# Kernel optimization log

Measured on AMD Instinct MI355X. Metric: run time of the kernel, lower is better.

## Reference

```python
import jax, jax.numpy as jnp
import numpy as np

NEG_SLOPE = 0.02

def setup_inputs() -> dict:
    key = jax.random.key(0)
    ks = jax.random.split(key, 6)
    B, C, H, W = 32, 64, 128, 128
    K, L, OUT = 1000, 12, 24
    x = jax.random.normal(ks[0], (B, C, H, W), dtype=jnp.float32)
    pos = jax.random.randint(ks[1], (K, B, L, 2), 0, 128, dtype=jnp.int32)
    # middle: Conv2d(C, C, 3, stride=1, padding=1)
    conv_w = jax.random.normal(ks[2], (C, C, 3, 3), dtype=jnp.float32) * (1.0 / np.sqrt(C * 9))
    conv_b = jax.random.normal(ks[3], (C,), dtype=jnp.float32) * 0.01
    # predictor: Linear(C*L, OUT), kaiming init, zero bias
    pred_w = jax.random.normal(ks[4], (OUT, C * L), dtype=jnp.float32) * np.sqrt(2.0 / (C * L))
    pred_b = jnp.zeros((OUT,), dtype=jnp.float32)
    return {"x": x, "pos": pos, "conv_w": conv_w, "conv_b": conv_b, "pred_w": pred_w, "pred_b": pred_b}

def reference(x, pos, conv_w, conv_b, pred_w, pred_b):
    # middle conv (3x3, same padding) + LeakyReLU(0.02)
    h = jax.lax.conv_general_dilated(
        x, conv_w, window_strides=(1, 1), padding=((1, 1), (1, 1)),
        dimension_numbers=("NCHW", "OIHW", "NCHW")) + conv_b[None, :, None, None]
    h = jnp.where(h > 0, h, NEG_SLOPE * h)  # [B,C,H,W]
    B, C, H, W = h.shape
    K, _, L, _ = pos.shape
    # clamp coords and build flattened spatial indices
    px = jnp.clip(pos[..., 0], 0, W - 1)
    py = jnp.clip(pos[..., 1], 0, H - 1)
    idx = (py * W + px).transpose(1, 0, 2)           # [B,K,L]
    hf = h.reshape(B, C, H * W).transpose(0, 2, 1)   # [B,HW,C]
    # irregular gather: per-batch pick L spatial locations for K candidates
    kernel_seq = hf[jnp.arange(B)[:, None, None], idx]  # [B,K,L,C]
    kernel_seq = kernel_seq.reshape(B, K, L * C)
    out = kernel_seq @ pred_w.T + pred_b             # [B,K,OUT]
    return out.transpose(1, 0, 2)                    # [K,B,OUT]
```

## Files before the change

kernel.cpp:

```cpp
#include <hip/hip_runtime.h>
#include <hip/hip_bf16.h>

typedef __attribute__((ext_vector_type(8))) short short8;
typedef __attribute__((ext_vector_type(4))) float f32x4;

#define NEG_SLOPE 0.02f

static __device__ __forceinline__ unsigned short f2bf(float f) {
    unsigned int u = __float_as_uint(f);
    u += 0x7fffu + ((u >> 16) & 1u);
    return (unsigned short)(u >> 16);
}

static __device__ __forceinline__ unsigned int pk2bf(float lo, float hi) {
    __hip_bfloat162 t = __float22bfloat162_rn(float2{lo, hi});
    unsigned int u;
    __builtin_memcpy(&u, &t, 4);
    return u;
}

__global__ __launch_bounds__(256) void prep_kernel(const float* __restrict__ conv_w,
                                                   const float* __restrict__ pred_w,
                                                   unsigned short* __restrict__ wb,
                                                   unsigned short* __restrict__ pwb) {
    int i = blockIdx.x * 256 + threadIdx.x;
    if (i < 36864) {
        int ci5 = i & 31, tap = (i >> 5) % 9, rest = i / 288;
        int co = rest & 63, cc = rest >> 6;
        int ci = cc * 32 + ci5;
        wb[i] = f2bf(conv_w[(co * 64 + ci) * 9 + tap]);
    }
    if (i < 24576) {
        int o = i / 768, k = i - o * 768;
        pwb[i] = f2bf(o < 24 ? pred_w[o * 768 + k] : 0.0f);
    }
}

#define ROW_BYTES 8320
#define WROW 304
__global__ __launch_bounds__(512, 4) void conv_mfma(const float* __restrict__ x,
                                                    const unsigned short* __restrict__ wb,
                                                    const float* __restrict__ cb,
                                                    unsigned short* __restrict__ h) {
    __shared__ unsigned short w_sm[64 * WROW];
    __shared__ unsigned char in_sm[4 * ROW_BYTES];

    const int id = blockIdx.x;
    const int xcd = id & 7, local = id >> 3;
    const int b = local & 31;
    const int y0 = ((xcd << 3) + (local >> 5)) * 2;

    const int tid = threadIdx.x;
    const int wave = tid >> 6, lane = tid & 63;
    const int lr = lane & 15, kg = lane >> 4;
    const int ro = wave >> 2;
    const int px0 = (wave & 3) * 32;

    f32x4 acc[2][4];
#pragma unroll
    for (int m = 0; m < 2; ++m)
#pragma unroll
        for (int n = 0; n < 4; ++n) acc[m][n] = (f32x4){0.f, 0.f, 0.f, 0.f};

    const unsigned char* ab[2][3];
#pragma unroll
    for (int m = 0; m < 2; ++m)
#pragma unroll
        for (int dx = 0; dx < 3; ++dx) {
            int xx = px0 + m * 16 + lr + dx;
            int pair = xx >> 1, odd = xx & 1;
            int slot = ((odd << 2) | kg) ^ (pair & 7);
            ab[m][dx] = in_sm + pair * 128 + slot * 16;
        }
    const unsigned short* bbp[4];
#pragma unroll
    for (int n = 0; n < 4; ++n) bbp[n] = w_sm + (n * 16 + lr) * WROW + kg * 8;

    const int s_pair = wave * 8 + (lane >> 3);
    const int s_odd = (lane >> 2) & 1, s_q = lane & 3;
    const int s_xx = s_pair * 2 + s_odd;
    const int s_gx = s_xx - 1;
    const int s_gxc = s_gx < 0 ? 0 : s_gx;
    const int s_slot = ((s_odd << 2) | s_q) ^ (s_pair & 7);
    const int s_dst = s_pair * 128 + s_slot * 16;

    for (int cc = 0; cc < 2; ++cc) {
        __syncthreads();
        const unsigned short* wsrc = wb + cc * 18432;
        for (int j = tid; j < 2304; j += 512) {
            int q = j & 3, tap = (j >> 2) % 9, co = j / 36;
            *(uint4*)(w_sm + co * WROW + tap * 32 + q * 8) = *(const uint4*)(wsrc + j * 8);
        }
        const float* xc = x + ((size_t)b * 64 + cc * 32 + s_q * 8) * 16384;
#pragma unroll
        for (int r = 0; r < 4; ++r) {
            int gy = y0 + r - 1;
            uint4 d = {0u, 0u, 0u, 0u};
            if ((unsigned)gy < 128u) {
                const float* src = xc + gy * 128 + s_gxc;
                float f[8];
#pragma unroll
                for (int c = 0; c < 8; ++c) f[c] = src[(size_t)c * 16384];
                if (s_gx >= 0) {
                    d.x = pk2bf(f[0], f[1]); d.y = pk2bf(f[2], f[3]);
                    d.z = pk2bf(f[4], f[5]); d.w = pk2bf(f[6], f[7]);
                }
            }
            *(uint4*)(in_sm + r * ROW_BYTES + s_dst) = d;
        }
        if (tid < 32) {
            int q = tid & 3, odd = (tid >> 2) & 1, r = tid >> 3;
            int gy = y0 + r - 1;
            uint4 d = {0u, 0u, 0u, 0u};
            if (odd == 0 && (unsigned)gy < 128u) {
                const float* src = x + ((size_t)b * 64 + cc * 32 + q * 8) * 16384 + gy * 128 + 127;
                float f[8];
#pragma unroll
                for (int c = 0; c < 8; ++c) f[c] = src[(size_t)c * 16384];
                d.x = pk2bf(f[0], f[1]); d.y = pk2bf(f[2], f[3]);
                d.z = pk2bf(f[4], f[5]); d.w = pk2bf(f[6], f[7]);
            }
            int slot = ((odd << 2) | q);
            *(uint4*)(in_sm + r * ROW_BYTES + 64 * 128 + slot * 16) = d;
        }
        __syncthreads();

#pragma unroll
        for (int t = 0; t < 9; ++t) {
            const int dy = t / 3, dx = t % 3;
            const int aoff = (ro + dy) * ROW_BYTES;
            short8 A0 = *(const short8*)(ab[0][dx] + aoff);
            short8 A1 = *(const short8*)(ab[1][dx] + aoff);
#pragma unroll
            for (int n = 0; n < 4; ++n) {
                short8 B = *(const short8*)(bbp[n] + t * 32);
                acc[0][n] = __builtin_amdgcn_mfma_f32_16x16x32_bf16(A0, B, acc[0][n], 0, 0, 0);
                acc[1][n] = __builtin_amdgcn_mfma_f32_16x16x32_bf16(A1, B, acc[1][n], 0, 0, 0);
            }
        }
    }

    float bias[4];
#pragma unroll
    for (int n = 0; n < 4; ++n) bias[n] = cb[n * 16 + lr];
    const int y = y0 + ro;
    const size_t hrow = (size_t)(b * 128 + y) * 128;
#pragma unroll
    for (int m = 0; m < 2; ++m)
#pragma unroll
        for (int rr = 0; rr < 4; ++rr) {
            const int p = px0 + m * 16 + kg * 4 + rr;
            unsigned short* hp = h + (hrow + p) * 64 + lr;
#pragma unroll
            for (int n = 0; n < 4; ++n) {
                float v = acc[m][n][rr] + bias[n];
                v = v > 0.0f ? v : NEG_SLOPE * v;
                hp[n * 16] = f2bf(v);
            }
        }
}

__global__ __launch_bounds__(256) void gather_gemm(const unsigned short* __restrict__ h,
                                                   const int* __restrict__ pos,
                                                   const unsigned short* __restrict__ pw,
                                                   const float* __restrict__ pred_b,
                                                   float* __restrict__ out) {
    __shared__ unsigned char pw_lds[32 * 1536];
    const int tid = threadIdx.x;

    for (int i = tid; i < 3072; i += 256) {
        int row = i / 96, c = i - row * 96;
        int dst = row * 1536 + ((c * 16) ^ ((row & 7) << 4));
        *(uint4*)(pw_lds + dst) = ((const uint4*)pw)[i];
    }
    __syncthreads();

    const int wave = tid >> 6, lane = tid & 63;
    const int pair_base = blockIdx.x * 64 + wave * 16;
    const int prow = lane & 15;
    const int kgrp = lane >> 4;
    const int pair = pair_base + prow;
    const int b = pair & 31;
    const unsigned short* hb = h + (size_t)b * 16384 * 64;

    const int swz0 = (prow & 7) << 4;
    const unsigned char* bro0 = pw_lds + prow * 1536;
    const unsigned char* bro1 = pw_lds + (prow + 16) * 1536;

    f32x4 acc0 = {0.f, 0.f, 0.f, 0.f};
    f32x4 acc1 = {0.f, 0.f, 0.f, 0.f};

#pragma unroll
    for (int l = 0; l < 12; ++l) {
        int2 pq = ((const int2*)pos)[pair * 12 + l];
        int px = pq.x < 0 ? 0 : (pq.x > 127 ? 127 : pq.x);
        int py = pq.y < 0 ? 0 : (pq.y > 127 ? 127 : pq.y);
        const unsigned short* pix = hb + (((size_t)py << 7) + px) * 64;
#pragma unroll
        for (int half = 0; half < 2; ++half) {
            const int c0 = half * 32 + kgrp * 8;
            short8 a = *(const short8*)(pix + c0);
            const int kb = (l * 64 + half * 32 + kgrp * 8) * 2;
            short8 b0 = *(const short8*)(bro0 + (kb ^ swz0));
            short8 b1 = *(const short8*)(bro1 + (kb ^ swz0));
            acc0 = __builtin_amdgcn_mfma_f32_16x16x32_bf16(a, b0, acc0, 0, 0, 0);
            acc1 = __builtin_amdgcn_mfma_f32_16x16x32_bf16(a, b1, acc1, 0, 0, 0);
        }
    }

    const int o0 = lane & 15;
    const float bias0 = pred_b[o0];
    const float bias1 = (o0 + 16 < 24) ? pred_b[o0 + 16] : 0.0f;
#pragma unroll
    for (int r = 0; r < 4; ++r) {
        const int pout = pair_base + (lane >> 4) * 4 + r;
        out[(size_t)pout * 24 + o0] = acc0[r] + bias0;
        if (o0 + 16 < 24)
            out[(size_t)pout * 24 + o0 + 16] = acc1[r] + bias1;
    }
}

extern "C" void kernel_launch(void* const* d_in, const int* in_sizes, int n_in,
                              void* d_out, int out_size, void* d_ws, size_t ws_size,
                              hipStream_t stream) {
    const float* x      = (const float*)d_in[0];
    const int*   pos    = (const int*)d_in[1];
    const float* conv_w = (const float*)d_in[2];
    const float* conv_b = (const float*)d_in[3];
    const float* pred_w = (const float*)d_in[4];
    const float* pred_b = (const float*)d_in[5];
    float* out = (float*)d_out;

    char* ws = (char*)d_ws;
    unsigned short* h   = (unsigned short*)ws;
    unsigned short* wb  = (unsigned short*)(ws + 67108864);
    unsigned short* pwb = (unsigned short*)(ws + 67108864 + 73728);

    prep_kernel<<<144, 256, 0, stream>>>(conv_w, pred_w, wb, pwb);
    conv_mfma<<<2048, 512, 0, stream>>>(x, wb, conv_b, h);
    gather_gemm<<<500, 256, 0, stream>>>(h, pos, pwb, pred_b, out);
}
```

Before: 88.08 us.

## Switch conv to 32x32x16 MFMA with padded weight layout and vectorized input staging

Replaces the 16x16x32 bf16 MFMA tiling in the conv with 32x32x16 MFMAs, so each wave computes 32 pixels by 64 output channels using two 16-register accumulators. The prep kernel now writes conv weights already padded to the shared-memory row stride (300), so weight staging becomes a straight contiguous copy. Input staging loads float2 pairs so each thread fills two pixel slots, and the halo columns are simply zeroed. The intent is fewer LDS reads per FLOP and cheaper global loads, at the cost of a different LDS bank-conflict pattern and output store layout.

Result: slower. 180.9 us (+105.4%).

```diff
diff --git a/kernel.cpp b/kernel.cpp
--- a/kernel.cpp
+++ b/kernel.cpp
@@ -3,6 +3,7 @@
 
 typedef __attribute__((ext_vector_type(8))) short short8;
 typedef __attribute__((ext_vector_type(4))) float f32x4;
+typedef __attribute__((ext_vector_type(16))) float f32x16;
 
 #define NEG_SLOPE 0.02f
 
@@ -19,16 +20,24 @@
     return u;
 }
 
+#define WROW 300
+#define ROW_BYTES 8320
+
 __global__ __launch_bounds__(256) void prep_kernel(const float* __restrict__ conv_w,
                                                    const float* __restrict__ pred_w,
                                                    unsigned short* __restrict__ wb,
                                                    unsigned short* __restrict__ pwb) {
     int i = blockIdx.x * 256 + threadIdx.x;
-    if (i < 36864) {
-        int ci5 = i & 31, tap = (i >> 5) % 9, rest = i / 288;
-        int co = rest & 63, cc = rest >> 6;
-        int ci = cc * 32 + ci5;
-        wb[i] = f2bf(conv_w[(co * 64 + ci) * 9 + tap]);
+    if (i < 2 * 64 * WROW) {
+        int cc = i / (64 * WROW);
+        int rem = i - cc * (64 * WROW);
+        int co = rem / WROW, e = rem - co * WROW;
+        float v = 0.0f;
+        if (e < 288) {
+            int tap = e >> 5, ci5 = e & 31;
+            v = conv_w[(co * 64 + cc * 32 + ci5) * 9 + tap];
+        }
+        wb[i] = f2bf(v);
     }
     if (i < 24576) {
         int o = i / 768, k = i - o * 768;
@@ -36,8 +45,6 @@
     }
 }
 
-#define ROW_BYTES 8320
-#define WROW 304
 __global__ __launch_bounds__(512, 4) void conv_mfma(const float* __restrict__ x,
                                                     const unsigned short* __restrict__ wb,
                                                     const float* __restrict__ cb,
@@ -52,76 +59,68 @@
 
     const int tid = threadIdx.x;
     const int wave = tid >> 6, lane = tid & 63;
-    const int lr = lane & 15, kg = lane >> 4;
+    const int l31 = lane & 31, hi = lane >> 5;
     const int ro = wave >> 2;
     const int px0 = (wave & 3) * 32;
-
-    f32x4 acc[2][4];
-#pragma unroll
-    for (int m = 0; m < 2; ++m)
-#pragma unroll
-        for (int n = 0; n < 4; ++n) acc[m][n] = (f32x4){0.f, 0.f, 0.f, 0.f};
-
-    const unsigned char* ab[2][3];
-#pragma unroll
-    for (int m = 0; m < 2; ++m)
-#pragma unroll
-        for (int dx = 0; dx < 3; ++dx) {
-            int xx = px0 + m * 16 + lr + dx;
-            int pair = xx >> 1, odd = xx & 1;
-            int slot = ((odd << 2) | kg) ^ (pair & 7);
-            ab[m][dx] = in_sm + pair * 128 + slot * 16;
-        }
-    const unsigned short* bbp[4];
-#pragma unroll
-    for (int n = 0; n < 4; ++n) bbp[n] = w_sm + (n * 16 + lr) * WROW + kg * 8;
-
-    const int s_pair = wave * 8 + (lane >> 3);
-    const int s_odd = (lane >> 2) & 1, s_q = lane & 3;
-    const int s_xx = s_pair * 2 + s_odd;
-    const int s_gx = s_xx - 1;
-    const int s_gxc = s_gx < 0 ? 0 : s_gx;
-    const int s_slot = ((s_odd << 2) | s_q) ^ (s_pair & 7);
-    const int s_dst = s_pair * 128 + s_slot * 16;
+    const int y = y0 + ro;
+
+    f32x16 acc[2];
+#pragma unroll
+    for (int n = 0; n < 2; ++n)
+#pragma unroll
+        for (int e = 0; e < 16; ++e) acc[n][e] = 0.0f;
+
+    const unsigned char* ab[3][2];
+#pragma unroll
+    for (int dx = 0; dx < 3; ++dx)
+#pragma unroll
+        for (int ks = 0; ks < 2; ++ks) {
+            int xx = px0 + l31 + dx;
+            int q = ks * 2 + hi;
+            int slot = (((xx & 1) << 2) | q) ^ ((xx >> 1) & 7);
+            ab[dx][ks] = in_sm + (xx >> 1) * 128 + slot * 16;
+        }
+    const unsigned short* bbp[2][2];
+#pragma unroll
+    for (int n = 0; n < 2; ++n)
+#pragma unroll
+        for (int ks = 0; ks < 2; ++ks)
+            bbp[n][ks] = w_sm + (n * 32 + l31) * WROW + ks * 16 + hi * 8;
+
+    const int p_ = tid & 63, q_ = (tid >> 6) & 3, rr_ = tid >> 8;
+    const int slotA = (4 | q_) ^ (p_ & 7);
+    const int dstA = p_ * 128 + slotA * 16;
+    const int slotB = q_ ^ ((p_ + 1) & 7);
+    const int dstB = (p_ + 1) * 128 + slotB * 16;
 
     for (int cc = 0; cc < 2; ++cc) {
         __syncthreads();
-        const unsigned short* wsrc = wb + cc * 18432;
-        for (int j = tid; j < 2304; j += 512) {
-            int q = j & 3, tap = (j >> 2) % 9, co = j / 36;
-            *(uint4*)(w_sm + co * WROW + tap * 32 + q * 8) = *(const uint4*)(wsrc + j * 8);
-        }
-        const float* xc = x + ((size_t)b * 64 + cc * 32 + s_q * 8) * 16384;
-#pragma unroll
-        for (int r = 0; r < 4; ++r) {
-            int gy = y0 + r - 1;
-            uint4 d = {0u, 0u, 0u, 0u};
+        const unsigned short* wsrc = wb + cc * (64 * WROW);
+        for (int j = tid; j < 2400; j += 512)
+            *(uint4*)(w_sm + j * 8) = *(const uint4*)(wsrc + j * 8);
+        const float* xq = x + ((size_t)b * 64 + cc * 32 + q_ * 8) * 16384;
+#pragma unroll
+        for (int pass = 0; pass < 2; ++pass) {
+            const int r = pass * 2 + rr_;
+            const int gy = y0 + r - 1;
+            uint4 A = {0u, 0u, 0u, 0u}, Bv = {0u, 0u, 0u, 0u};
             if ((unsigned)gy < 128u) {
-                const float* src = xc + gy * 128 + s_gxc;
-                float f[8];
-#pragma unroll
-                for (int c = 0; c < 8; ++c) f[c] = src[(size_t)c * 16384];
-                if (s_gx >= 0) {
-                    d.x = pk2bf(f[0], f[1]); d.y = pk2bf(f[2], f[3]);
-                    d.z = pk2bf(f[4], f[5]); d.w = pk2bf(f[6], f[7]);
-                }
+                const float* src = xq + gy * 128 + 2 * p_;
+                float2 f[8];
+#pragma unroll
+                for (int c = 0; c < 8; ++c) f[c] = *(const float2*)(src + (size_t)c * 16384);
+                A.x = pk2bf(f[0].x, f[1].x); A.y = pk2bf(f[2].x, f[3].x);
+                A.z = pk2bf(f[4].x, f[5].x); A.w = pk2bf(f[6].x, f[7].x);
+                Bv.x = pk2bf(f[0].y, f[1].y); Bv.y = pk2bf(f[2].y, f[3].y);
+                Bv.z = pk2bf(f[4].y, f[5].y); Bv.w = pk2bf(f[6].y, f[7].y);
             }
-            *(uint4*)(in_sm + r * ROW_BYTES + s_dst) = d;
+            *(uint4*)(in_sm + r * ROW_BYTES + dstA) = A;
+            *(uint4*)(in_sm + r * ROW_BYTES + dstB) = Bv;
         }
         if (tid < 32) {
-            int q = tid & 3, odd = (tid >> 2) & 1, r = tid >> 3;
-            int gy = y0 + r - 1;
-            uint4 d = {0u, 0u, 0u, 0u};
-            if (odd == 0 && (unsigned)gy < 128u) {
-                const float* src = x + ((size_t)b * 64 + cc * 32 + q * 8) * 16384 + gy * 128 + 127;
-                float f[8];
-#pragma unroll
-                for (int c = 0; c < 8; ++c) f[c] = src[(size_t)c * 16384];
-                d.x = pk2bf(f[0], f[1]); d.y = pk2bf(f[2], f[3]);
-                d.z = pk2bf(f[4], f[5]); d.w = pk2bf(f[6], f[7]);
-            }
-            int slot = ((odd << 2) | q);
-            *(uint4*)(in_sm + r * ROW_BYTES + 64 * 128 + slot * 16) = d;
+            int q = tid & 3, r = (tid >> 2) & 3, which = tid >> 4;
+            int dst = which == 0 ? (q * 16) : (64 * 128 + (4 | q) * 16);
+            *(uint4*)(in_sm + r * ROW_BYTES + dst) = (uint4){0u, 0u, 0u, 0u};
         }
         __syncthreads();
 
@@ -129,34 +128,30 @@
         for (int t = 0; t < 9; ++t) {
             const int dy = t / 3, dx = t % 3;
             const int aoff = (ro + dy) * ROW_BYTES;
-            short8 A0 = *(const short8*)(ab[0][dx] + aoff);
-            short8 A1 = *(const short8*)(ab[1][dx] + aoff);
-#pragma unroll
-            for (int n = 0; n < 4; ++n) {
-                short8 B = *(const short8*)(bbp[n] + t * 32);
-                acc[0][n] = __builtin_amdgcn_mfma_f32_16x16x32_bf16(A0, B, acc[0][n], 0, 0, 0);
-                acc[1][n] = __builtin_amdgcn_mfma_f32_16x16x32_bf16(A1, B, acc[1][n], 0, 0, 0);
+            short8 A0 = *(const short8*)(ab[dx][0] + aoff);
+            short8 A1 = *(const short8*)(ab[dx][1] + aoff);
+#pragma unroll
+            for (int n = 0; n < 2; ++n) {
+                short8 B0 = *(const short8*)(bbp[n][0] + t * 32);
+                short8 B1 = *(const short8*)(bbp[n][1] + t * 32);
+                acc[n] = __builtin_amdgcn_mfma_f32_32x32x16_bf16(A0, B0, acc[n], 0, 0, 0);
+                acc[n] = __builtin_amdgcn_mfma_f32_32x32x16_bf16(A1, B1, acc[n], 0, 0, 0);
             }
         }
     }
 
-    float bias[4];
-#pragma unroll
-    for (int n = 0; n < 4; ++n) bias[n] = cb[n * 16 + lr];
-    const int y = y0 + ro;
+    float bias[2];
+#pragma unroll
+    for (int n = 0; n < 2; ++n) bias[n] = cb[n * 32 + l31];
     const size_t hrow = (size_t)(b * 128 + y) * 128;
 #pragma unroll
-    for (int m = 0; m < 2; ++m)
-#pragma unroll
-        for (int rr = 0; rr < 4; ++rr) {
-            const int p = px0 + m * 16 + kg * 4 + rr;
-            unsigned short* hp = h + (hrow + p) * 64 + lr;
-#pragma unroll
-            for (int n = 0; n < 4; ++n) {
-                float v = acc[m][n][rr] + bias[n];
-                v = v > 0.0f ? v : NEG_SLOPE * v;
-                hp[n * 16] = f2bf(v);
-            }
+    for (int n = 0; n < 2; ++n)
+#pragma unroll
+        for (int reg = 0; reg < 16; ++reg) {
+            const int px = px0 + (reg & 3) + 8 * (reg >> 2) + 4 * hi;
+            float v = acc[n][reg] + bias[n];
+            v = v > 0.0f ? v : NEG_SLOPE * v;
+            h[(hrow + px) * 64 + n * 32 + l31] = f2bf(v);
         }
 }
 
@@ -234,9 +229,9 @@
     char* ws = (char*)d_ws;
     unsigned short* h   = (unsigned short*)ws;
     unsigned short* wb  = (unsigned short*)(ws + 67108864);
-    unsigned short* pwb = (unsigned short*)(ws + 67108864 + 73728);
-
-    prep_kernel<<<144, 256, 0, stream>>>(conv_w, pred_w, wb, pwb);
+    unsigned short* pwb = (unsigned short*)(ws + 67108864 + 76800);
+
+    prep_kernel<<<160, 256, 0, stream>>>(conv_w, pred_w, wb, pwb);
     conv_mfma<<<2048, 512, 0, stream>>>(x, wb, conv_b, h);
     gather_gemm<<<500, 256, 0, stream>>>(h, pos, pwb, pred_b, out);
 }
```

## Prefetch second channel chunk during compute, vectorize input loads, pre-pad conv weights

Applied to the files above, without the earlier changes.

The conv kernel now issues the global loads for the second 32-channel chunk into registers before computing on the first chunk, so memory latency can overlap the MFMA work. Input rows are loaded as float2 pairs and split into even and odd pixel slots, replacing scalar loads and removing the separate halo load path. Border columns are zeroed explicitly instead. The prep kernel writes weights already padded to the shared-memory row stride, so staging becomes a flat vector copy. The extra in-flight registers may reduce occupancy.

Result: faster. 86.04 us (-2.3%).

```diff
diff --git a/kernel.cpp b/kernel.cpp
--- a/kernel.cpp
+++ b/kernel.cpp
@@ -19,16 +19,24 @@
     return u;
 }
 
+#define WROW 304
+#define ROW_BYTES 8320
+
 __global__ __launch_bounds__(256) void prep_kernel(const float* __restrict__ conv_w,
                                                    const float* __restrict__ pred_w,
                                                    unsigned short* __restrict__ wb,
                                                    unsigned short* __restrict__ pwb) {
     int i = blockIdx.x * 256 + threadIdx.x;
-    if (i < 36864) {
-        int ci5 = i & 31, tap = (i >> 5) % 9, rest = i / 288;
-        int co = rest & 63, cc = rest >> 6;
-        int ci = cc * 32 + ci5;
-        wb[i] = f2bf(conv_w[(co * 64 + ci) * 9 + tap]);
+    if (i < 2 * 64 * WROW) {
+        int cc = i / (64 * WROW);
+        int rem = i - cc * (64 * WROW);
+        int co = rem / WROW, e = rem - co * WROW;
+        float v = 0.0f;
+        if (e < 288) {
+            int tap = e >> 5, ci5 = e & 31;
+            v = conv_w[(co * 64 + cc * 32 + ci5) * 9 + tap];
+        }
+        wb[i] = f2bf(v);
     }
     if (i < 24576) {
         int o = i / 768, k = i - o * 768;
@@ -36,8 +44,6 @@
     }
 }
 
-#define ROW_BYTES 8320
-#define WROW 304
 __global__ __launch_bounds__(512, 4) void conv_mfma(const float* __restrict__ x,
                                                     const unsigned short* __restrict__ wb,
                                                     const float* __restrict__ cb,
@@ -55,6 +61,7 @@
     const int lr = lane & 15, kg = lane >> 4;
     const int ro = wave >> 2;
     const int px0 = (wave & 3) * 32;
+    const int y = y0 + ro;
 
     f32x4 acc[2][4];
 #pragma unroll
@@ -76,74 +83,104 @@
 #pragma unroll
     for (int n = 0; n < 4; ++n) bbp[n] = w_sm + (n * 16 + lr) * WROW + kg * 8;
 
-    const int s_pair = wave * 8 + (lane >> 3);
-    const int s_odd = (lane >> 2) & 1, s_q = lane & 3;
-    const int s_xx = s_pair * 2 + s_odd;
-    const int s_gx = s_xx - 1;
-    const int s_gxc = s_gx < 0 ? 0 : s_gx;
-    const int s_slot = ((s_odd << 2) | s_q) ^ (s_pair & 7);
-    const int s_dst = s_pair * 128 + s_slot * 16;
-
-    for (int cc = 0; cc < 2; ++cc) {
-        __syncthreads();
-        const unsigned short* wsrc = wb + cc * 18432;
-        for (int j = tid; j < 2304; j += 512) {
-            int q = j & 3, tap = (j >> 2) % 9, co = j / 36;
-            *(uint4*)(w_sm + co * WROW + tap * 32 + q * 8) = *(const uint4*)(wsrc + j * 8);
-        }
-        const float* xc = x + ((size_t)b * 64 + cc * 32 + s_q * 8) * 16384;
-#pragma unroll
-        for (int r = 0; r < 4; ++r) {
-            int gy = y0 + r - 1;
-            uint4 d = {0u, 0u, 0u, 0u};
-            if ((unsigned)gy < 128u) {
-                const float* src = xc + gy * 128 + s_gxc;
-                float f[8];
-#pragma unroll
-                for (int c = 0; c < 8; ++c) f[c] = src[(size_t)c * 16384];
-                if (s_gx >= 0) {
-                    d.x = pk2bf(f[0], f[1]); d.y = pk2bf(f[2], f[3]);
-                    d.z = pk2bf(f[4], f[5]); d.w = pk2bf(f[6], f[7]);
-                }
-            }
-            *(uint4*)(in_sm + r * ROW_BYTES + s_dst) = d;
-        }
-        if (tid < 32) {
-            int q = tid & 3, odd = (tid >> 2) & 1, r = tid >> 3;
-            int gy = y0 + r - 1;
-            uint4 d = {0u, 0u, 0u, 0u};
-            if (odd == 0 && (unsigned)gy < 128u) {
-                const float* src = x + ((size_t)b * 64 + cc * 32 + q * 8) * 16384 + gy * 128 + 127;
-                float f[8];
-#pragma unroll
-                for (int c = 0; c < 8; ++c) f[c] = src[(size_t)c * 16384];
-                d.x = pk2bf(f[0], f[1]); d.y = pk2bf(f[2], f[3]);
-                d.z = pk2bf(f[4], f[5]); d.w = pk2bf(f[6], f[7]);
-            }
-            int slot = ((odd << 2) | q);
-            *(uint4*)(in_sm + r * ROW_BYTES + 64 * 128 + slot * 16) = d;
-        }
-        __syncthreads();
-
-#pragma unroll
-        for (int t = 0; t < 9; ++t) {
-            const int dy = t / 3, dx = t % 3;
-            const int aoff = (ro + dy) * ROW_BYTES;
-            short8 A0 = *(const short8*)(ab[0][dx] + aoff);
-            short8 A1 = *(const short8*)(ab[1][dx] + aoff);
-#pragma unroll
-            for (int n = 0; n < 4; ++n) {
-                short8 B = *(const short8*)(bbp[n] + t * 32);
-                acc[0][n] = __builtin_amdgcn_mfma_f32_16x16x32_bf16(A0, B, acc[0][n], 0, 0, 0);
-                acc[1][n] = __builtin_amdgcn_mfma_f32_16x16x32_bf16(A1, B, acc[1][n], 0, 0, 0);
-            }
-        }
-    }
+    const int p_ = tid & 63, q_ = (tid >> 6) & 3, rr_ = tid >> 8;
+    const int slotA = (4 | q_) ^ (p_ & 7);
+    const int dstA = p_ * 128 + slotA * 16;
+    const int slotB = q_ ^ ((p_ + 1) & 7);
+    const int dstB = (p_ + 1) * 128 + slotB * 16;
+
+    float2 F[2][8];
+
+#define LOADX(CCI)                                                                 \
+    {                                                                              \
+        const float* xq_ = x + ((size_t)b * 64 + (CCI) * 32 + q_ * 8) * 16384;     \
+        _Pragma("unroll")                                                          \
+        for (int pass = 0; pass < 2; ++pass) {                                     \
+            const int r_ = pass * 2 + rr_;                                         \
+            const int gy_ = y0 + r_ - 1;                                           \
+            if ((unsigned)gy_ < 128u) {                                            \
+                const float* s_ = xq_ + gy_ * 128 + 2 * p_;                        \
+                _Pragma("unroll")                                                  \
+                for (int c = 0; c < 8; ++c)                                        \
+                    F[pass][c] = *(const float2*)(s_ + (size_t)c * 16384);         \
+            } else {                                                               \
+                _Pragma("unroll")                                                  \
+                for (int c = 0; c < 8; ++c) F[pass][c] = (float2){0.f, 0.f};       \
+            }                                                                      \
+        }                                                                          \
+    }
+
+#define STOREX()                                                                   \
+    {                                                                              \
+        _Pragma("unroll")                                                          \
+        for (int pass = 0; pass < 2; ++pass) {                                     \
+            const int r_ = pass * 2 + rr_;                                         \
+            uint4 Av, Bv;                                                          \
+            Av.x = pk2bf(F[pass][0].x, F[pass][1].x);                              \
+            Av.y = pk2bf(F[pass][2].x, F[pass][3].x);                              \
+            Av.z = pk2bf(F[pass][4].x, F[pass][5].x);                              \
+            Av.w = pk2bf(F[pass][6].x, F[pass][7].x);                              \
+            Bv.x = pk2bf(F[pass][0].y, F[pass][1].y);                              \
+            Bv.y = pk2bf(F[pass][2].y, F[pass][3].y);                              \
+            Bv.z = pk2bf(F[pass][4].y, F[pass][5].y);                              \
+            Bv.w = pk2bf(F[pass][6].y, F[pass][7].y);                              \
+            *(uint4*)(in_sm + r_ * ROW_BYTES + dstA) = Av;                         \
+            *(uint4*)(in_sm + r_ * ROW_BYTES + dstB) = Bv;                         \
+        }                                                                          \
+    }
+
+#define STAGEW(CCI)                                                                \
+    {                                                                              \
+        const unsigned short* wsrc_ = wb + (CCI) * (64 * WROW);                    \
+        for (int j = tid; j < 2432; j += 512)                                      \
+            *(uint4*)(w_sm + j * 8) = *(const uint4*)(wsrc_ + j * 8);              \
+    }
+
+#define TAILZ()                                                                    \
+    if (tid < 32) {                                                                \
+        int q = tid & 3, r = (tid >> 2) & 3, which = tid >> 4;                     \
+        int dst = which == 0 ? (q * 16) : (64 * 128 + (4 | q) * 16);               \
+        *(uint4*)(in_sm + r * ROW_BYTES + dst) = (uint4){0u, 0u, 0u, 0u};          \
+    }
+
+#define COMPUTE()                                                                  \
+    _Pragma("unroll")                                                              \
+    for (int t = 0; t < 9; ++t) {                                                  \
+        const int dy = t / 3, dx = t % 3;                                          \
+        const int aoff = (ro + dy) * ROW_BYTES;                                    \
+        short8 A0 = *(const short8*)(ab[0][dx] + aoff);                            \
+        short8 A1 = *(const short8*)(ab[1][dx] + aoff);                            \
+        _Pragma("unroll")                                                          \
+        for (int n = 0; n < 4; ++n) {                                              \
+            short8 B = *(const short8*)(bbp[n] + t * 32);                          \
+            acc[0][n] = __builtin_amdgcn_mfma_f32_16x16x32_bf16(A0, B, acc[0][n], 0, 0, 0); \
+            acc[1][n] = __builtin_amdgcn_mfma_f32_16x16x32_bf16(A1, B, acc[1][n], 0, 0, 0); \
+        }                                                                          \
+    }
+
+    LOADX(0)
+    STAGEW(0)
+    STOREX()
+    TAILZ()
+    LOADX(1)
+    __syncthreads();
+    COMPUTE()
+    __syncthreads();
+    STAGEW(1)
+    STOREX()
+    TAILZ()
+    __syncthreads();
+    COMPUTE()
+
+#undef LOADX
+#undef STOREX
+#undef STAGEW
+#undef TAILZ
+#undef COMPUTE
 
     float bias[4];
 #pragma unroll
     for (int n = 0; n < 4; ++n) bias[n] = cb[n * 16 + lr];
-    const int y = y0 + ro;
     const size_t hrow = (size_t)(b * 128 + y) * 128;
 #pragma unroll
     for (int m = 0; m < 2; ++m)
@@ -234,9 +271,9 @@
     char* ws = (char*)d_ws;
     unsigned short* h   = (unsigned short*)ws;
     unsigned short* wb  = (unsigned short*)(ws + 67108864);
-    unsigned short* pwb = (unsigned short*)(ws + 67108864 + 73728);
-
-    prep_kernel<<<144, 256, 0, stream>>>(conv_w, pred_w, wb, pwb);
+    unsigned short* pwb = (unsigned short*)(ws + 67108864 + 77824);
+
+    prep_kernel<<<152, 256, 0, stream>>>(conv_w, pred_w, wb, pwb);
     conv_mfma<<<2048, 512, 0, stream>>>(x, wb, conv_b, h);
     gather_gemm<<<500, 256, 0, stream>>>(h, pos, pwb, pred_b, out);
 }
```
